# Kernel optimization log

Hardware: AMD Instinct MI355X
Metric: run time of the kernel (lower is better)

The kernel has to match this reference:

```python
import jax, jax.numpy as jnp
import numpy as np

BINS = 10
MMT = 0.9
N = 33554432  # 2^25 elements


def setup_inputs() -> dict:
    key = jax.random.key(0)
    k1, k2, k3 = jax.random.split(key, 3)
    pred = jax.random.normal(k1, (N,), dtype=jnp.float32)
    target = jax.random.randint(k2, (N,), 0, 2, dtype=jnp.int32)
    acc_sum = jax.random.uniform(k3, (BINS,), dtype=jnp.float32)
    return {"pred": pred, "target": target, "acc_sum": acc_sum}


def reference(pred, target, acc_sum):
    bins = acc_sum.shape[0]
    # border = arange(bins+1)/bins, with last edge nudged up by 1e-6
    border = jnp.arange(bins + 1, dtype=jnp.float32) / bins
    border = border.at[-1].add(1e-6)

    t = target.astype(jnp.float32)
    # gradient density measure on detached predictions
    g = jnp.abs(jax.nn.sigmoid(jax.lax.stop_gradient(pred)) - t)
    # bin index: g in [border[i], border[i+1])  ->  i
    idx = jnp.clip(jnp.searchsorted(border, g, side='right') - 1, 0, bins - 1)

    # single-pass histogram (replaces the per-bin mask loop)
    counts = jax.ops.segment_sum(jnp.ones_like(g), idx, num_segments=bins)
    nonempty = counts > 0

    # momentum-accumulated bin statistics (only updated for non-empty bins)
    acc_new = jnp.where(nonempty, MMT * acc_sum + (1.0 - MMT) * counts, acc_sum)

    tot = jnp.float32(max(pred.shape[0], 1.0))
    safe_acc = jnp.where(nonempty, acc_new, 1.0)
    bin_w = jnp.where(nonempty, tot / safe_acc, 0.0)  # [bins]

    n = jnp.sum(nonempty.astype(jnp.float32))
    bin_w = jnp.where(n > 0, bin_w / jnp.maximum(n, 1.0), bin_w)

    # per-element GHM weights are constants w.r.t. pred (buffer + detached g)
    w = jax.lax.stop_gradient(bin_w[idx])

    # BCE-with-logits, numerically stable
    bce = jnp.maximum(pred, 0.0) - pred * t + jnp.log1p(jnp.exp(-jnp.abs(pred)))
    return jnp.sum(w * bce) / tot
```

## Files before the change

kernel.cpp:

```cpp
#include <hip/hip_runtime.h>

#define BINS 10
#define NTHREADS 256
#define LOG2E 1.44269504f
#define KBIAS 1024.0f
#define TILE_ELEMS (NTHREADS * 64)
#define ROUND_BYTES (NTHREADS * 16)


typedef float        f32x4 __attribute__((ext_vector_type(4)));
typedef unsigned int u32x4 __attribute__((ext_vector_type(4)));

__device__ __forceinline__ float wave_reduce_add(float v) {
#pragma unroll
    for (int off = 32; off > 0; off >>= 1) v += __shfl_down(v, off, 64);
    return v;
}
__device__ __forceinline__ unsigned int wave_reduce_addu(unsigned int v) {
#pragma unroll
    for (int off = 32; off > 0; off >>= 1) v += __shfl_down((int)v, off, 64);
    return v;
}

__global__ __launch_bounds__(NTHREADS, 6) void ghm_pass1(
    const float* __restrict__ pred, const int* __restrict__ target,
    float* __restrict__ g_T,
    unsigned int* __restrict__ g_C,
    int n)
{
    float T0 = 0.f;
    float Tb[9];
#pragma unroll
    for (int b = 0; b < 9; ++b) Tb[b] = 0.f;

    const int tid    = threadIdx.x;
    const int ntiles = n / TILE_ELEMS;

#define GHM_ELEM(x_, tu_)                                                   \
    {                                                                       \
        const float z = (x_) * LOG2E;                                       \
        const float w = ((tu_) != 0u) ? z : -z;                             \
        const float E = __builtin_amdgcn_exp2f(-w);                         \
        const float bce2 = __builtin_amdgcn_logf(1.0f + E);                 \
        const float ad = bce2 + KBIAS;                                      \
        T0 += bce2;                                                         \
        Tb[0] += (w <=  3.16992500f) ? ad : 0.f;                            \
        Tb[1] += (w <=  2.0f)        ? ad : 0.f;                            \
        Tb[2] += (w <=  1.22239242f) ? ad : 0.f;                            \
        Tb[3] += (w <=  0.58496250f) ? ad : 0.f;                            \
        Tb[4] += (w <=  0.0f)        ? ad : 0.f;                            \
        Tb[5] += (w <= -0.58496250f) ? ad : 0.f;                            \
        Tb[6] += (w <= -1.22239242f) ? ad : 0.f;                            \
        Tb[7] += (w <= -2.0f)        ? ad : 0.f;                            \
        Tb[8] += (w <= -3.16992500f) ? ad : 0.f;                            \
    }

#define COMPUTE(X, Tv)                                                      \
    {                                                                       \
        GHM_ELEM((X)[0], (Tv)[0]); GHM_ELEM((X)[1], (Tv)[1]);               \
        GHM_ELEM((X)[2], (Tv)[2]); GHM_ELEM((X)[3], (Tv)[3]);               \
    }

#define ISSUE(X, Tv, off)                                                   \
    asm volatile("global_load_dwordx4 %0, %2, %3\n\t"                       \
                 "global_load_dwordx4 %1, %2, %4"                           \
                 : "=&v"(X), "=&v"(Tv)                                      \
                 : "v"(off), "s"(pred), "s"(target))

#define VWAIT(nn)                                                           \
    do { asm volatile("s_waitcnt vmcnt(" #nn ")" ::: "memory");             \
         __builtin_amdgcn_sched_barrier(0); } while (0)

    if (blockIdx.x < (unsigned)ntiles) {
        unsigned int voff = (unsigned)blockIdx.x * (TILE_ELEMS * 4u)
                          + (unsigned)tid * 16u;
        f32x4 x0, x1, x2, x3;
        u32x4 t0, t1, t2, t3;

        ISSUE(x0, t0, voff); voff += ROUND_BYTES;
        ISSUE(x1, t1, voff); voff += ROUND_BYTES;
        ISSUE(x2, t2, voff); voff += ROUND_BYTES;
        ISSUE(x3, t3, voff); voff += ROUND_BYTES;

#pragma unroll 1
        for (int g = 0; g < 3; ++g) {
            VWAIT(6); COMPUTE(x0, t0); ISSUE(x0, t0, voff); voff += ROUND_BYTES;
            VWAIT(6); COMPUTE(x1, t1); ISSUE(x1, t1, voff); voff += ROUND_BYTES;
            VWAIT(6); COMPUTE(x2, t2); ISSUE(x2, t2, voff); voff += ROUND_BYTES;
            VWAIT(6); COMPUTE(x3, t3); ISSUE(x3, t3, voff); voff += ROUND_BYTES;
        }
        VWAIT(6); COMPUTE(x0, t0);
        VWAIT(4); COMPUTE(x1, t1);
        VWAIT(2); COMPUTE(x2, t2);
        VWAIT(0); COMPUTE(x3, t3);
    }

    if (blockIdx.x == gridDim.x - 1) {
        for (int i = ntiles * TILE_ELEMS + tid; i < n; i += NTHREADS) {
            const float xs = pred[i];
            const unsigned int tu = (unsigned int)target[i];
            GHM_ELEM(xs, tu);
        }
    }
#undef ISSUE
#undef VWAIT
#undef COMPUTE
#undef GHM_ELEM

    float        sums[BINS];
    unsigned int cnts[BINS];
    sums[0] = T0; cnts[0] = 0u;
#pragma unroll
    for (int b = 1; b < BINS; ++b) {
        const float cf = floorf(Tb[b - 1] * (1.0f / KBIAS));
        cnts[b] = (unsigned int)cf;
        sums[b] = Tb[b - 1] - KBIAS * cf;
    }

    __shared__ float        r_T[BINS];
    __shared__ unsigned int r_C[BINS];
    if (tid < BINS) { r_T[tid] = 0.f; r_C[tid] = 0u; }
    __syncthreads();

    const int lane = tid & 63;
#pragma unroll
    for (int b = 0; b < BINS; ++b) {
        const float        v = wave_reduce_add(sums[b]);
        const unsigned int c = (b > 0) ? wave_reduce_addu(cnts[b]) : 0u;
        if (lane == 0) {
            atomicAdd(&r_T[b], v);
            if (b > 0) atomicAdd(&r_C[b], c);
        }
    }
    __syncthreads();

    if (tid < BINS) {
        atomicAdd(&g_T[tid], r_T[tid]);
        atomicAdd(&g_C[tid], r_C[tid]);
    }
}

__global__ void ghm_finalize(const float* __restrict__ g_T,
                             const unsigned int* __restrict__ g_C,
                             const float* __restrict__ acc_sum,
                             float* __restrict__ out, float tot, unsigned int ntot)
{
    if (threadIdx.x == 0 && blockIdx.x == 0) {
        const float LN2 = 0.69314718056f;
        float S[BINS];
        float cntf[BINS];
#pragma unroll
        for (int b = 0; b < BINS; ++b) {
            const float        Tc = g_T[b];
            const float        Tn = (b + 1 < BINS) ? g_T[b + 1] : 0.f;
            const unsigned int Cc = (b == 0) ? ntot : g_C[b];
            const unsigned int Cn = (b + 1 < BINS) ? g_C[b + 1] : 0u;
            S[b]    = (Tc - Tn) * LN2;
            cntf[b] = (float)(Cc - Cn);
        }
        float binw[BINS];
        int nne = 0;
#pragma unroll
        for (int b = 0; b < BINS; ++b) {
            const bool ne = (cntf[b] > 0.0f);
            const float accn = ne ? (0.9f * acc_sum[b] + 0.1f * cntf[b]) : acc_sum[b];
            binw[b] = ne ? (tot / accn) : 0.0f;
            nne += ne ? 1 : 0;
        }
        const float scale = (nne > 0) ? (1.0f / (float)nne) : 1.0f;
        float res = 0.0f;
#pragma unroll
        for (int b = 0; b < BINS; ++b) res += (binw[b] * scale) * S[b];
        out[0] = res / tot;
    }
}

extern "C" void kernel_launch(void* const* d_in, const int* in_sizes, int n_in,
                              void* d_out, int out_size, void* d_ws, size_t ws_size,
                              hipStream_t stream) {
    const float* pred    = (const float*)d_in[0];
    const int*   target  = (const int*)d_in[1];
    const float* acc_sum = (const float*)d_in[2];
    float*       out     = (float*)d_out;

    const int n = in_sizes[0];
    const int ntiles = n / TILE_ELEMS;
    const int grid = (ntiles > 0) ? ntiles : 1;

    float*        g_T = (float*)d_ws;
    unsigned int* g_C = (unsigned int*)((float*)d_ws + BINS);

    hipMemsetAsync(d_ws, 0, 2 * BINS * sizeof(float), stream);

    ghm_pass1<<<grid, NTHREADS, 0, stream>>>(pred, target, g_T, g_C, n);

    const float tot = (float)(n > 1 ? n : 1);
    ghm_finalize<<<1, 64, 0, stream>>>(g_T, g_C, acc_sum, out, tot, (unsigned int)n);
}
```

Measured before the change: 84.05 us.

## Replace global atomics and memset with per-block partials and reduce kernel

Each block now writes its 10 bin sums and 10 counts to a per-block row in the workspace instead of doing global atomic adds. The finalize kernel is replaced by a reduction kernel that sums all rows before computing the loss. This removes the memset launch and atomic contention on a few addresses. In exchange it adds a serial partial-sum reduction in one block, and counts are now carried as floats.

```diff
diff --git a/kernel.cpp b/kernel.cpp
--- a/kernel.cpp
+++ b/kernel.cpp
@@ -6,6 +6,7 @@
 #define KBIAS 1024.0f
 #define TILE_ELEMS (NTHREADS * 64)
 #define ROUND_BYTES (NTHREADS * 16)
+#define PCOLS 20
 
 
 typedef float        f32x4 __attribute__((ext_vector_type(4)));
@@ -24,8 +25,7 @@
 
 __global__ __launch_bounds__(NTHREADS, 6) void ghm_pass1(
     const float* __restrict__ pred, const int* __restrict__ target,
-    float* __restrict__ g_T,
-    unsigned int* __restrict__ g_C,
+    float* __restrict__ part,
     int n)
 {
     float T0 = 0.f;
@@ -134,29 +134,47 @@
     }
     __syncthreads();
 
-    if (tid < BINS) {
-        atomicAdd(&g_T[tid], r_T[tid]);
-        atomicAdd(&g_C[tid], r_C[tid]);
-    }
-}
-
-__global__ void ghm_finalize(const float* __restrict__ g_T,
-                             const unsigned int* __restrict__ g_C,
-                             const float* __restrict__ acc_sum,
-                             float* __restrict__ out, float tot, unsigned int ntot)
+    if (tid < PCOLS) {
+        const float v = (tid < BINS) ? r_T[tid] : (float)r_C[tid - BINS];
+        part[blockIdx.x * PCOLS + tid] = v;
+    }
+}
+
+__global__ void ghm_reduce(const float* __restrict__ part,
+                           const float* __restrict__ acc_sum,
+                           float* __restrict__ out, float tot,
+                           unsigned int ntot, int rows)
 {
-    if (threadIdx.x == 0 && blockIdx.x == 0) {
+    __shared__ float s[PCOLS][12];
+    const int tid = threadIdx.x;
+    const int c = tid % PCOLS;
+    const int g = tid / PCOLS;
+    if (g < 12) {
+        float acc = 0.f;
+        for (int r = g; r < rows; r += 12) acc += part[r * PCOLS + c];
+        s[c][g] = acc;
+    }
+    __syncthreads();
+
+    if (tid == 0) {
         const float LN2 = 0.69314718056f;
-        float S[BINS];
-        float cntf[BINS];
+        float T[BINS];
+        float Cc[BINS];
 #pragma unroll
         for (int b = 0; b < BINS; ++b) {
-            const float        Tc = g_T[b];
-            const float        Tn = (b + 1 < BINS) ? g_T[b + 1] : 0.f;
-            const unsigned int Cc = (b == 0) ? ntot : g_C[b];
-            const unsigned int Cn = (b + 1 < BINS) ? g_C[b + 1] : 0u;
-            S[b]    = (Tc - Tn) * LN2;
-            cntf[b] = (float)(Cc - Cn);
+            float ts = 0.f, cs = 0.f;
+            for (int gg = 0; gg < 12; ++gg) { ts += s[b][gg]; cs += s[b + BINS][gg]; }
+            T[b] = ts; Cc[b] = cs;
+        }
+        Cc[0] = (float)ntot;
+
+        float S[BINS], cntf[BINS];
+#pragma unroll
+        for (int b = 0; b < BINS; ++b) {
+            const float Tn = (b + 1 < BINS) ? T[b + 1]  : 0.f;
+            const float Cn = (b + 1 < BINS) ? Cc[b + 1] : 0.f;
+            S[b]    = (T[b] - Tn) * LN2;
+            cntf[b] = Cc[b] - Cn;
         }
         float binw[BINS];
         int nne = 0;
@@ -187,13 +205,11 @@
     const int ntiles = n / TILE_ELEMS;
     const int grid = (ntiles > 0) ? ntiles : 1;
 
-    float*        g_T = (float*)d_ws;
-    unsigned int* g_C = (unsigned int*)((float*)d_ws + BINS);
-
-    hipMemsetAsync(d_ws, 0, 2 * BINS * sizeof(float), stream);
-
-    ghm_pass1<<<grid, NTHREADS, 0, stream>>>(pred, target, g_T, g_C, n);
+    float* part = (float*)d_ws;
+
+    ghm_pass1<<<grid, NTHREADS, 0, stream>>>(pred, target, part, n);
 
     const float tot = (float)(n > 1 ? n : 1);
-    ghm_finalize<<<1, 64, 0, stream>>>(g_T, g_C, acc_sum, out, tot, (unsigned int)n);
-}
+    ghm_reduce<<<1, NTHREADS, 0, stream>>>(part, acc_sum, out, tot,
+                                           (unsigned int)n, grid);
+}
```

Measured after the change: 96.65 us. 1.15x slower.
